# Performance work log

Measured on AMD Instinct MI355X. Metric: run time of the kernel, lower is better.

## Reference

```python
import jax, jax.numpy as jnp
import numpy as np

B, N, D, K, DSPACE, NFREQ = 4, 4096, 256, 16, 3, 5
BN_EPS = 1e-5


def setup_inputs() -> dict:
    key = jax.random.key(0)
    ks = jax.random.split(key, 12)
    s = 1.0 / np.sqrt(D)
    pe_in = DSPACE * 2 * NFREQ + DSPACE  # 33
    return {
        "xyz": jax.random.normal(ks[0], (B, N, DSPACE), jnp.float32),
        "feats": jax.random.normal(ks[1], (B, N, D), jnp.float32),
        "w_q": jax.random.uniform(ks[2], (D, D), jnp.float32, -s, s),
        "w_k": jax.random.uniform(ks[3], (D, D), jnp.float32, -s, s),
        "w_v": jax.random.uniform(ks[4], (D, D), jnp.float32, -s, s),
        "g_w1": jax.random.uniform(ks[5], (D, D), jnp.float32, -s, s),
        "g_b1": jax.random.uniform(ks[6], (D,), jnp.float32, -s, s),
        "g_w2": jax.random.uniform(ks[7], (D, D), jnp.float32, -s, s),
        "g_b2": jax.random.uniform(ks[8], (D,), jnp.float32, -s, s),
        "pe_w": jax.random.uniform(ks[9], (D, pe_in), jnp.float32, -s, s),
        "pe_b": jax.random.uniform(ks[10], (D,), jnp.float32, -s, s),
        "bn_w": jnp.ones((D,), jnp.float32),
        "bn_b": jnp.zeros((D,), jnp.float32),
    }


def _gather_knn(points, idx):
    # points [b,n,c], idx [b,n,k] -> [b,n,k,c]
    return jax.vmap(lambda p, i: p[i])(points, idx)


def reference(xyz, feats, w_q, w_k, w_v, g_w1, g_b1, g_w2, g_b2, pe_w, pe_b, bn_w, bn_b):
    # KNN (no grad in original): full pairwise sq-distance + top-k smallest
    dists = jnp.sum((xyz[:, :, None] - xyz[:, None]) ** 2, axis=-1)  # [b,n,n]
    _, knn_idx = jax.lax.top_k(-dists, K)  # [b,n,k], ascending distance
    knn_idx = jax.lax.stop_gradient(knn_idx)
    knn_xyz = jax.lax.stop_gradient(_gather_knn(xyz, knn_idx))  # [b,n,k,3]

    q = feats @ w_q.T                               # [b,n,d]
    k_g = _gather_knn(feats @ w_k.T, knn_idx)       # [b,n,k,d]
    v_g = _gather_knn(feats @ w_v.T, knn_idx)       # [b,n,k,d]

    pos_diff = xyz[:, :, None] - knn_xyz            # [b,n,k,3]
    freqs = jnp.linspace(1.0, 2.0 ** NFREQ, NFREQ).astype(pos_diff.dtype)
    embeds = [pos_diff]
    for f in freqs:
        embeds.append(jnp.sin(pos_diff * f))
        embeds.append(jnp.cos(pos_diff * f))
    pos_embed = jnp.concatenate(embeds, axis=-1)    # [b,n,k,33]
    pos_encode = pos_embed @ pe_w.T + pe_b          # [b,n,k,d]

    edges = q[:, :, None] - k_g + pos_encode        # [b,n,k,d]
    h = jax.nn.relu(edges @ g_w1.T + g_b1)
    attn = h @ g_w2.T + g_b2                        # [b,n,k,d]
    attn = jax.nn.softmax(attn, axis=-2)            # softmax over neighbors

    res = jnp.einsum('bnkf,bnkf->bnf', attn, v_g + pos_encode) + feats

    # BatchNorm1d over channel dim, training-mode batch stats (biased var)
    mean = jnp.mean(res, axis=(0, 1))
    var = jnp.var(res, axis=(0, 1))
    res = (res - mean) * jax.lax.rsqrt(var + BN_EPS) * bn_w + bn_b
    return res
```

## Files before the change

### kernel.cpp

```cpp
#include <hip/hip_runtime.h>

#define BB 4
#define NN 4096
#define DD 256
#define KK 16
#define PTS 2

typedef __bf16 bf16;
typedef __attribute__((ext_vector_type(8))) __bf16 bf16x8;
typedef __attribute__((ext_vector_type(4))) __bf16 bf16x4;
typedef __attribute__((ext_vector_type(4))) float f32x4;

__global__ __launch_bounds__(256) void prep_kernel(
    const float* __restrict__ wq, const float* __restrict__ wk,
    const float* __restrict__ wv, const float* __restrict__ w1,
    const float* __restrict__ w2, const float* __restrict__ pw,
    bf16* __restrict__ wqb, bf16* __restrict__ wkb, bf16* __restrict__ wvb,
    bf16* __restrict__ w1b, bf16* __restrict__ w2b, bf16* __restrict__ pwb) {
  const int idx = blockIdx.x * 256 + threadIdx.x;
  wqb[idx] = (bf16)wq[idx];
  wkb[idx] = (bf16)wk[idx];
  wvb[idx] = (bf16)wv[idx];
  w1b[idx] = (bf16)w1[idx];
  w2b[idx] = (bf16)w2[idx];
  if (idx < 256 * 64) {
    const int n = idx >> 6, c = idx & 63;
    pwb[idx] = (c < 33) ? (bf16)pw[n * 33 + c] : (bf16)0.f;
  }
}

__global__ __launch_bounds__(256, 2) void knn_v2(const float* __restrict__ xyz,
                                                 int* __restrict__ knn) {
  const int lane = threadIdx.x & 63;
  const int wv = threadIdx.x >> 6;
  const int row = blockIdx.x * 4 + wv;
  const int b = row >> 12, i = row & (NN - 1);
  const float* xb = xyz + (size_t)b * NN * 3;
  const float xi = xb[i * 3 + 0], yi = xb[i * 3 + 1], zi = xb[i * 3 + 2];
  unsigned long long cand[64];
#pragma unroll
  for (int c = 0; c < 64; ++c) {
    const int j = c * 64 + lane;
    const float dx = xi - xb[j * 3 + 0];
    const float dy = yi - xb[j * 3 + 1];
    const float dz = zi - xb[j * 3 + 2];
    const float d = dx * dx + dy * dy + dz * dz;
    const unsigned long long fb = (unsigned long long)(__float_as_uint(d)) + 1ull;
    cand[c] = (fb << 32) | (unsigned int)j;
  }
  unsigned long long lastkey = 0ull;
  unsigned int myj = 0u;
  for (int r = 0; r < KK; ++r) {
    unsigned long long lmin = ~0ull;
#pragma unroll
    for (int c = 0; c < 64; ++c) {
      const unsigned long long v = cand[c];
      if (v > lastkey && v < lmin) lmin = v;
    }
#pragma unroll
    for (int off = 1; off < 64; off <<= 1) {
      const unsigned long long o = __shfl_xor(lmin, off);
      if (o < lmin) lmin = o;
    }
    if (lane == r) myj = (unsigned int)lmin;
    lastkey = lmin;
  }
  if (lane < KK) knn[row * KK + lane] = (int)myj;
}

__global__ __launch_bounds__(256, 4) void proj_mfma(
    const float* __restrict__ feats, const bf16* __restrict__ wqb,
    const bf16* __restrict__ wkb, const bf16* __restrict__ wvb,
    float* __restrict__ q, bf16* __restrict__ kfb, bf16* __restrict__ vfb) {
  const int t = threadIdx.x;
  const int lane = t & 63, wv = t >> 6;
  const int m = lane & 15, qd = lane >> 4;
  const size_t r0 = (size_t)blockIdx.x * 64;
  __shared__ __align__(16) bf16 fs[64][264];
  const float4* f4 = (const float4*)(feats + r0 * DD);
  for (int i = 0; i < 16; ++i) {
    const int e = i * 256 + t;
    const float4 v = f4[e];
    bf16x4 w;
    w[0] = (bf16)v.x; w[1] = (bf16)v.y; w[2] = (bf16)v.z; w[3] = (bf16)v.w;
    *(bf16x4*)&fs[e >> 6][(e & 63) * 4] = w;
  }
  __syncthreads();
  bf16x8 afrag[8];
#pragma unroll
  for (int f = 0; f < 8; ++f)
    afrag[f] = *(const bf16x8*)&fs[wv * 16 + m][f * 32 + qd * 8];
  const bf16* wmat[3] = {wqb, wkb, wvb};
  for (int mat = 0; mat < 3; ++mat) {
    const bf16* wb = wmat[mat];
    for (int nt = 0; nt < 16; ++nt) {
      const int n = nt * 16 + m;
      bf16x8 bfr[8];
#pragma unroll
      for (int f = 0; f < 8; ++f)
        bfr[f] = *(const bf16x8*)(wb + (size_t)n * DD + f * 32 + qd * 8);
      f32x4 c = {0.f, 0.f, 0.f, 0.f};
#pragma unroll
      for (int f = 0; f < 8; ++f)
        c = __builtin_amdgcn_mfma_f32_16x16x32_bf16(afrag[f], bfr[f], c, 0, 0, 0);
#pragma unroll
      for (int rr = 0; rr < 4; ++rr) {
        const size_t o = (r0 + wv * 16 + qd * 4 + rr) * DD + n;
        if (mat == 0) q[o] = c[rr];
        else if (mat == 1) kfb[o] = (bf16)c[rr];
        else vfb[o] = (bf16)c[rr];
      }
    }
  }
}

__global__ __launch_bounds__(256, 3) void edge_v3(
    const float* __restrict__ xyz, const float* __restrict__ feats,
    const float* __restrict__ q, const bf16* __restrict__ kfb,
    const bf16* __restrict__ vfb, const int* __restrict__ knn,
    const bf16* __restrict__ w1b, const float* __restrict__ g_b1,
    const bf16* __restrict__ w2b, const float* __restrict__ g_b2,
    const bf16* __restrict__ pwb, const float* __restrict__ pe_b,
    float* __restrict__ res) {
  const int t = threadIdx.x;
  const int lane = t & 63;
  const int wv = t >> 6;
  const int m = lane & 15;
  const int qd = lane >> 4;
  const int row0 = blockIdx.x * PTS;
  const int b = row0 >> 12;

  __shared__ __align__(16) bf16 emb_s[PTS][16][88];
  __shared__ __align__(16) bf16 bufA[PTS][16][264];
  __shared__ __align__(16) bf16 bufB[PTS][16][264];
  __shared__ int js_s[PTS][16];

  if (t < PTS * 16) js_s[t >> 4][t & 15] = knn[(row0 + (t >> 4)) * KK + (t & 15)];
  __syncthreads();

  const float* xb = xyz + (size_t)b * NN * 3;
  for (int p = 0; p < PTS; ++p) {
    const int i = (row0 + p) & (NN - 1);
    for (int e = t; e < 16 * 88; e += 256) {
      const int k = e / 88, c = e % 88;
      float val = 0.f;
      if (c < 33) {
        const int cc = (c < 3) ? c : (c - 3) % 3;
        const float pd = xb[i * 3 + cc] - xb[js_s[p][k] * 3 + cc];
        if (c < 3) {
          val = pd;
        } else {
          const int f = (c - 3) / 6;
          const float x = pd * fmaf(7.75f, (float)f, 1.0f);
          val = (((c - 3) % 6) < 3) ? __sinf(x) : __cosf(x);
        }
      }
      emb_s[p][k][c] = (bf16)val;
    }
  }
  __syncthreads();

  float vpe[4][PTS][4];
#pragma unroll
  for (int tt = 0; tt < 4; ++tt) {
    const int n = wv * 64 + tt * 16 + m;
    const bf16x8 b0 = *(const bf16x8*)(pwb + (size_t)n * 64 + qd * 8);
    const bf16x8 b1 = *(const bf16x8*)(pwb + (size_t)n * 64 + 32 + qd * 8);
    const float bias = pe_b[n];
#pragma unroll
    for (int p = 0; p < PTS; ++p) {
      const bf16x8 a0 = *(const bf16x8*)&emb_s[p][m][qd * 8];
      const bf16x8 a1 = *(const bf16x8*)&emb_s[p][m][32 + qd * 8];
      f32x4 c = {bias, bias, bias, bias};
      c = __builtin_amdgcn_mfma_f32_16x16x32_bf16(a0, b0, c, 0, 0, 0);
      c = __builtin_amdgcn_mfma_f32_16x16x32_bf16(a1, b1, c, 0, 0, 0);
      const float qv = q[(size_t)(row0 + p) * DD + n];
#pragma unroll
      for (int rr = 0; rr < 4; ++rr) {
        const int krow = qd * 4 + rr;
        const size_t jr = ((size_t)(b * NN + js_s[p][krow])) * DD + n;
        bufA[p][krow][n] = (bf16)(qv - (float)kfb[jr] + c[rr]);
        vpe[tt][p][rr] = (float)vfb[jr] + c[rr];
      }
    }
  }
  __syncthreads();

  {
    bf16x8 afrag[PTS][8];
#pragma unroll
    for (int p = 0; p < PTS; ++p)
#pragma unroll
      for (int f = 0; f < 8; ++f)
        afrag[p][f] = *(const bf16x8*)&bufA[p][m][f * 32 + qd * 8];
    for (int tt = 0; tt < 4; ++tt) {
      const int n = wv * 64 + tt * 16 + m;
      bf16x8 bfr[8];
#pragma unroll
      for (int f = 0; f < 8; ++f)
        bfr[f] = *(const bf16x8*)(w1b + (size_t)n * DD + f * 32 + qd * 8);
      const float bias = g_b1[n];
#pragma unroll
      for (int p = 0; p < PTS; ++p) {
        f32x4 c = {bias, bias, bias, bias};
#pragma unroll
        for (int f = 0; f < 8; ++f)
          c = __builtin_amdgcn_mfma_f32_16x16x32_bf16(afrag[p][f], bfr[f], c, 0, 0, 0);
#pragma unroll
        for (int rr = 0; rr < 4; ++rr)
          bufB[p][qd * 4 + rr][n] = (bf16)fmaxf(c[rr], 0.f);
      }
    }
  }
  __syncthreads();

  {
    bf16x8 afrag[PTS][8];
#pragma unroll
    for (int p = 0; p < PTS; ++p)
#pragma unroll
      for (int f = 0; f < 8; ++f)
        afrag[p][f] = *(const bf16x8*)&bufB[p][m][f * 32 + qd * 8];
#pragma unroll
    for (int tt = 0; tt < 4; ++tt) {
      const int n = wv * 64 + tt * 16 + m;
      bf16x8 bfr[8];
#pragma unroll
      for (int f = 0; f < 8; ++f)
        bfr[f] = *(const bf16x8*)(w2b + (size_t)n * DD + f * 32 + qd * 8);
      const float bias = g_b2[n];
#pragma unroll
      for (int p = 0; p < PTS; ++p) {
        f32x4 c = {bias, bias, bias, bias};
#pragma unroll
        for (int f = 0; f < 8; ++f)
          c = __builtin_amdgcn_mfma_f32_16x16x32_bf16(afrag[p][f], bfr[f], c, 0, 0, 0);
        float mx = fmaxf(fmaxf(c[0], c[1]), fmaxf(c[2], c[3]));
        mx = fmaxf(mx, __shfl_xor(mx, 16));
        mx = fmaxf(mx, __shfl_xor(mx, 32));
        float e[4], den = 0.f;
#pragma unroll
        for (int rr = 0; rr < 4; ++rr) {
          e[rr] = __expf(c[rr] - mx);
          den += e[rr];
        }
        den += __shfl_xor(den, 16);
        den += __shfl_xor(den, 32);
        float num = 0.f;
#pragma unroll
        for (int rr = 0; rr < 4; ++rr) num += e[rr] * vpe[tt][p][rr];
        num += __shfl_xor(num, 16);
        num += __shfl_xor(num, 32);
        if (qd == 0) {
          const size_t o = (size_t)(row0 + p) * DD + n;
          res[o] = num / den + feats[o];
        }
      }
    }
  }
}

__global__ __launch_bounds__(256) void bn_stats(const float* __restrict__ res,
                                                float* __restrict__ sums,
                                                float* __restrict__ sumsq) {
  const int t = threadIdx.x;
  const size_t r0 = (size_t)blockIdx.x * 32;
  float s = 0.f, s2 = 0.f;
  for (int r = 0; r < 32; ++r) {
    const float v = res[(r0 + r) * DD + t];
    s += v;
    s2 += v * v;
  }
  atomicAdd(&sums[t], s);
  atomicAdd(&sumsq[t], s2);
}

__global__ __launch_bounds__(256) void bn_apply(float* __restrict__ out,
                                                const float* __restrict__ sums,
                                                const float* __restrict__ sumsq,
                                                const float* __restrict__ bn_w,
                                                const float* __restrict__ bn_b) {
  const int idx = blockIdx.x * 256 + threadIdx.x;
  const int c = idx & (DD - 1);
  const float inv_n = 1.f / (float)(BB * NN);
  const float mean = sums[c] * inv_n;
  const float var = sumsq[c] * inv_n - mean * mean;
  const float v = out[idx];
  out[idx] = (v - mean) * rsqrtf(var + 1e-5f) * bn_w[c] + bn_b[c];
}

extern "C" void kernel_launch(void* const* d_in, const int* in_sizes, int n_in,
                              void* d_out, int out_size, void* d_ws,
                              size_t ws_size, hipStream_t stream) {
  (void)in_sizes; (void)n_in; (void)out_size; (void)ws_size;
  const float* xyz = (const float*)d_in[0];
  const float* feats = (const float*)d_in[1];
  const float* w_q = (const float*)d_in[2];
  const float* w_k = (const float*)d_in[3];
  const float* w_v = (const float*)d_in[4];
  const float* g_w1 = (const float*)d_in[5];
  const float* g_b1 = (const float*)d_in[6];
  const float* g_w2 = (const float*)d_in[7];
  const float* g_b2 = (const float*)d_in[8];
  const float* pe_w = (const float*)d_in[9];
  const float* pe_b = (const float*)d_in[10];
  const float* bn_w = (const float*)d_in[11];
  const float* bn_b = (const float*)d_in[12];
  float* out = (float*)d_out;

  const int BN = BB * NN;
  char* w = (char*)d_ws;
  int* knn = (int*)w;       w += (size_t)BN * KK * 4;
  float* q = (float*)w;     w += (size_t)BN * DD * 4;
  bf16* kfb = (bf16*)w;     w += (size_t)BN * DD * 2;
  bf16* vfb = (bf16*)w;     w += (size_t)BN * DD * 2;
  float* sums = (float*)w;  w += DD * 4;
  float* sumsq = (float*)w; w += DD * 4;
  bf16* wqb = (bf16*)w;     w += (size_t)DD * DD * 2;
  bf16* wkb = (bf16*)w;     w += (size_t)DD * DD * 2;
  bf16* wvb = (bf16*)w;     w += (size_t)DD * DD * 2;
  bf16* w1b = (bf16*)w;     w += (size_t)DD * DD * 2;
  bf16* w2b = (bf16*)w;     w += (size_t)DD * DD * 2;
  bf16* pwb = (bf16*)w;     w += (size_t)DD * 64 * 2;

  prep_kernel<<<DD * DD / 256, 256, 0, stream>>>(w_q, w_k, w_v, g_w1, g_w2,
                                                 pe_w, wqb, wkb, wvb, w1b, w2b,
                                                 pwb);
  knn_v2<<<BN / 4, 256, 0, stream>>>(xyz, knn);
  proj_mfma<<<BN / 64, 256, 0, stream>>>(feats, wqb, wkb, wvb, q, kfb, vfb);
  edge_v3<<<BN / PTS, 256, 0, stream>>>(xyz, feats, q, kfb, vfb, knn, w1b, g_b1,
                                        w2b, g_b2, pwb, pe_b, out);
  hipMemsetAsync(sums, 0, 2 * DD * sizeof(float), stream);
  bn_stats<<<BN / 32, 256, 0, stream>>>(out, sums, sumsq);
  bn_apply<<<BN, 256, 0, stream>>>(out, sums, sumsq, bn_w, bn_b);
}
```

Before: 679.5 us.

## Prefetch gathered K/V rows into registers early and alias edge LDS buffers

The edge kernel now issues the gathered key and value loads right after reading the neighbour indices. Keys are loaded as row-contiguous bf16x8 MFMA A-fragments straight from global memory, and the q-k+pe subtraction happens in registers, so the bufA round trip is gone. The embedding buffer and the hidden-activation buffer share one LDS region, which cuts shared-memory use, and the sums memset moves into the prep kernel to drop one launch. In exchange, register pressure rises because the ab and vpe arrays stay live across the positional-encoding stage, which could reduce occupancy under launch_bounds(256,3).

New measurement: 762.6 us. 1.12x slower.

```diff
diff --git a/kernel.cpp b/kernel.cpp
--- a/kernel.cpp
+++ b/kernel.cpp
@@ -16,7 +16,8 @@
     const float* __restrict__ wv, const float* __restrict__ w1,
     const float* __restrict__ w2, const float* __restrict__ pw,
     bf16* __restrict__ wqb, bf16* __restrict__ wkb, bf16* __restrict__ wvb,
-    bf16* __restrict__ w1b, bf16* __restrict__ w2b, bf16* __restrict__ pwb) {
+    bf16* __restrict__ w1b, bf16* __restrict__ w2b, bf16* __restrict__ pwb,
+    float* __restrict__ sums) {
   const int idx = blockIdx.x * 256 + threadIdx.x;
   wqb[idx] = (bf16)wq[idx];
   wkb[idx] = (bf16)wk[idx];
@@ -27,6 +28,7 @@
     const int n = idx >> 6, c = idx & 63;
     pwb[idx] = (c < 33) ? (bf16)pw[n * 33 + c] : (bf16)0.f;
   }
+  if (idx < 2 * DD) sums[idx] = 0.f;
 }
 
 __global__ __launch_bounds__(256, 2) void knn_v2(const float* __restrict__ xyz,
@@ -114,7 +116,7 @@
   }
 }
 
-__global__ __launch_bounds__(256, 3) void edge_v3(
+__global__ __launch_bounds__(256, 3) void edge_v4(
     const float* __restrict__ xyz, const float* __restrict__ feats,
     const float* __restrict__ q, const bf16* __restrict__ kfb,
     const bf16* __restrict__ vfb, const int* __restrict__ knn,
@@ -130,37 +132,64 @@
   const int row0 = blockIdx.x * PTS;
   const int b = row0 >> 12;
 
-  __shared__ __align__(16) bf16 emb_s[PTS][16][88];
-  __shared__ __align__(16) bf16 bufA[PTS][16][264];
-  __shared__ __align__(16) bf16 bufB[PTS][16][264];
+  __shared__ __align__(16) bf16 peq_s[PTS][16][264];
+  __shared__ __align__(16) char un_s[PTS * 16 * 264 * 2];
+  bf16(*hs)[16][264] = (bf16(*)[16][264])un_s;
+  bf16(*emb_s)[16][96] = (bf16(*)[16][96])un_s;
   __shared__ int js_s[PTS][16];
 
   if (t < PTS * 16) js_s[t >> 4][t & 15] = knn[(row0 + (t >> 4)) * KK + (t & 15)];
   __syncthreads();
 
+  float vpe[4][PTS][4];
+#pragma unroll
+  for (int tt = 0; tt < 4; ++tt) {
+    const int n = wv * 64 + tt * 16 + m;
+#pragma unroll
+    for (int p = 0; p < PTS; ++p)
+#pragma unroll
+      for (int rr = 0; rr < 4; ++rr)
+        vpe[tt][p][rr] =
+            (float)vfb[((size_t)(b * NN + js_s[p][qd * 4 + rr])) * DD + n];
+  }
+  bf16x8 ab[PTS][8];
+#pragma unroll
+  for (int p = 0; p < PTS; ++p) {
+    const size_t base = ((size_t)(b * NN + js_s[p][m])) * DD;
+#pragma unroll
+    for (int f = 0; f < 8; ++f)
+      ab[p][f] = *(const bf16x8*)(kfb + base + f * 32 + qd * 8);
+  }
+
   const float* xb = xyz + (size_t)b * NN * 3;
-  for (int p = 0; p < PTS; ++p) {
-    const int i = (row0 + p) & (NN - 1);
-    for (int e = t; e < 16 * 88; e += 256) {
-      const int k = e / 88, c = e % 88;
-      float val = 0.f;
-      if (c < 33) {
-        const int cc = (c < 3) ? c : (c - 3) % 3;
-        const float pd = xb[i * 3 + cc] - xb[js_s[p][k] * 3 + cc];
-        if (c < 3) {
-          val = pd;
-        } else {
-          const int f = (c - 3) / 6;
-          const float x = pd * fmaf(7.75f, (float)f, 1.0f);
-          val = (((c - 3) % 6) < 3) ? __sinf(x) : __cosf(x);
+  {
+    const int k = t >> 4;
+    const int c0 = (t & 15) * 6;
+#pragma unroll
+    for (int p = 0; p < PTS; ++p) {
+      const int i = (row0 + p) & (NN - 1);
+      const int j = js_s[p][k];
+#pragma unroll
+      for (int cc = 0; cc < 6; ++cc) {
+        const int c = c0 + cc;
+        float val = 0.f;
+        if (c < 33) {
+          const int ax = (c < 3) ? c : (c - 3) % 3;
+          const float pd = xb[i * 3 + ax] - xb[j * 3 + ax];
+          if (c < 3) {
+            val = pd;
+          } else {
+            const int f = (c - 3) / 6;
+            const float x = pd * fmaf(7.75f, (float)f, 1.0f);
+            val = (((c - 3) % 6) < 3) ? __sinf(x) : __cosf(x);
+          }
         }
-      }
-      emb_s[p][k][c] = (bf16)val;
-    }
-  }
-  __syncthreads();
-
-  float vpe[4][PTS][4];
+        emb_s[p][k][c] = (bf16)val;
+      }
+    }
+  }
+  __syncthreads();
+
 #pragma unroll
   for (int tt = 0; tt < 4; ++tt) {
     const int n = wv * 64 + tt * 16 + m;
@@ -177,84 +206,82 @@
       const float qv = q[(size_t)(row0 + p) * DD + n];
 #pragma unroll
       for (int rr = 0; rr < 4; ++rr) {
-        const int krow = qd * 4 + rr;
-        const size_t jr = ((size_t)(b * NN + js_s[p][krow])) * DD + n;
-        bufA[p][krow][n] = (bf16)(qv - (float)kfb[jr] + c[rr]);
-        vpe[tt][p][rr] = (float)vfb[jr] + c[rr];
-      }
-    }
-  }
-  __syncthreads();
-
-  {
-    bf16x8 afrag[PTS][8];
-#pragma unroll
-    for (int p = 0; p < PTS; ++p)
+        peq_s[p][qd * 4 + rr][n] = (bf16)(c[rr] + qv);
+        vpe[tt][p][rr] += c[rr];
+      }
+    }
+  }
+  __syncthreads();
+
+#pragma unroll
+  for (int p = 0; p < PTS; ++p) {
+#pragma unroll
+    for (int f = 0; f < 8; ++f) {
+      const bf16x8 pq = *(const bf16x8*)&peq_s[p][m][f * 32 + qd * 8];
+      bf16x8 e;
+#pragma unroll
+      for (int x = 0; x < 8; ++x) e[x] = (bf16)((float)pq[x] - (float)ab[p][f][x]);
+      ab[p][f] = e;
+    }
+  }
+  for (int tt = 0; tt < 4; ++tt) {
+    const int n = wv * 64 + tt * 16 + m;
+    bf16x8 bfr[8];
+#pragma unroll
+    for (int f = 0; f < 8; ++f)
+      bfr[f] = *(const bf16x8*)(w1b + (size_t)n * DD + f * 32 + qd * 8);
+    const float bias = g_b1[n];
+#pragma unroll
+    for (int p = 0; p < PTS; ++p) {
+      f32x4 c = {bias, bias, bias, bias};
 #pragma unroll
       for (int f = 0; f < 8; ++f)
-        afrag[p][f] = *(const bf16x8*)&bufA[p][m][f * 32 + qd * 8];
-    for (int tt = 0; tt < 4; ++tt) {
-      const int n = wv * 64 + tt * 16 + m;
-      bf16x8 bfr[8];
+        c = __builtin_amdgcn_mfma_f32_16x16x32_bf16(ab[p][f], bfr[f], c, 0, 0, 0);
+#pragma unroll
+      for (int rr = 0; rr < 4; ++rr)
+        hs[p][qd * 4 + rr][n] = (bf16)fmaxf(c[rr], 0.f);
+    }
+  }
+  __syncthreads();
+
+#pragma unroll
+  for (int p = 0; p < PTS; ++p)
+#pragma unroll
+    for (int f = 0; f < 8; ++f)
+      ab[p][f] = *(const bf16x8*)&hs[p][m][f * 32 + qd * 8];
+#pragma unroll
+  for (int tt = 0; tt < 4; ++tt) {
+    const int n = wv * 64 + tt * 16 + m;
+    bf16x8 bfr[8];
+#pragma unroll
+    for (int f = 0; f < 8; ++f)
+      bfr[f] = *(const bf16x8*)(w2b + (size_t)n * DD + f * 32 + qd * 8);
+    const float bias = g_b2[n];
+#pragma unroll
+    for (int p = 0; p < PTS; ++p) {
+      f32x4 c = {bias, bias, bias, bias};
 #pragma unroll
       for (int f = 0; f < 8; ++f)
-        bfr[f] = *(const bf16x8*)(w1b + (size_t)n * DD + f * 32 + qd * 8);
-      const float bias = g_b1[n];
-#pragma unroll
-      for (int p = 0; p < PTS; ++p) {
-        f32x4 c = {bias, bias, bias, bias};
-#pragma unroll
-        for (int f = 0; f < 8; ++f)
-          c = __builtin_amdgcn_mfma_f32_16x16x32_bf16(afrag[p][f], bfr[f], c, 0, 0, 0);
-#pragma unroll
-        for (int rr = 0; rr < 4; ++rr)
-          bufB[p][qd * 4 + rr][n] = (bf16)fmaxf(c[rr], 0.f);
-      }
-    }
-  }
-  __syncthreads();
-
-  {
-    bf16x8 afrag[PTS][8];
-#pragma unroll
-    for (int p = 0; p < PTS; ++p)
-#pragma unroll
-      for (int f = 0; f < 8; ++f)
-        afrag[p][f] = *(const bf16x8*)&bufB[p][m][f * 32 + qd * 8];
-#pragma unroll
-    for (int tt = 0; tt < 4; ++tt) {
-      const int n = wv * 64 + tt * 16 + m;
-      bf16x8 bfr[8];
-#pragma unroll
-      for (int f = 0; f < 8; ++f)
-        bfr[f] = *(const bf16x8*)(w2b + (size_t)n * DD + f * 32 + qd * 8);
-      const float bias = g_b2[n];
-#pragma unroll
-      for (int p = 0; p < PTS; ++p) {
-        f32x4 c = {bias, bias, bias, bias};
-#pragma unroll
-        for (int f = 0; f < 8; ++f)
-          c = __builtin_amdgcn_mfma_f32_16x16x32_bf16(afrag[p][f], bfr[f], c, 0, 0, 0);
-        float mx = fmaxf(fmaxf(c[0], c[1]), fmaxf(c[2], c[3]));
-        mx = fmaxf(mx, __shfl_xor(mx, 16));
-        mx = fmaxf(mx, __shfl_xor(mx, 32));
-        float e[4], den = 0.f;
-#pragma unroll
-        for (int rr = 0; rr < 4; ++rr) {
-          e[rr] = __expf(c[rr] - mx);
-          den += e[rr];
-        }
-        den += __shfl_xor(den, 16);
-        den += __shfl_xor(den, 32);
-        float num = 0.f;
-#pragma unroll
-        for (int rr = 0; rr < 4; ++rr) num += e[rr] * vpe[tt][p][rr];
-        num += __shfl_xor(num, 16);
-        num += __shfl_xor(num, 32);
-        if (qd == 0) {
-          const size_t o = (size_t)(row0 + p) * DD + n;
-          res[o] = num / den + feats[o];
-        }
+        c = __builtin_amdgcn_mfma_f32_16x16x32_bf16(ab[p][f], bfr[f], c, 0, 0, 0);
+      float mx = fmaxf(fmaxf(c[0], c[1]), fmaxf(c[2], c[3]));
+      mx = fmaxf(mx, __shfl_xor(mx, 16));
+      mx = fmaxf(mx, __shfl_xor(mx, 32));
+      float e[4], den = 0.f;
+#pragma unroll
+      for (int rr = 0; rr < 4; ++rr) {
+        e[rr] = __expf(c[rr] - mx);
+        den += e[rr];
+      }
+      den += __shfl_xor(den, 16);
+      den += __shfl_xor(den, 32);
+      float num = 0.f;
+#pragma unroll
+      for (int rr = 0; rr < 4; ++rr) num += e[rr] * vpe[tt][p][rr];
+      num += __shfl_xor(num, 16);
+      num += __shfl_xor(num, 32);
+      if (qd == 0) {
+        const size_t o = (size_t)(row0 + p) * DD + n;
+        res[o] = num / den + feats[o];
       }
     }
   }
@@ -325,12 +352,11 @@
 
   prep_kernel<<<DD * DD / 256, 256, 0, stream>>>(w_q, w_k, w_v, g_w1, g_w2,
                                                  pe_w, wqb, wkb, wvb, w1b, w2b,
-                                                 pwb);
+                                                 pwb, sums);
   knn_v2<<<BN / 4, 256, 0, stream>>>(xyz, knn);
   proj_mfma<<<BN / 64, 256, 0, stream>>>(feats, wqb, wkb, wvb, q, kfb, vfb);
-  edge_v3<<<BN / PTS, 256, 0, stream>>>(xyz, feats, q, kfb, vfb, knn, w1b, g_b1,
+  edge_v4<<<BN / PTS, 256, 0, stream>>>(xyz, feats, q, kfb, vfb, knn, w1b, g_b1,
                                         w2b, g_b2, pwb, pe_b, out);
-  hipMemsetAsync(sums, 0, 2 * DD * sizeof(float), stream);
   bn_stats<<<BN / 32, 256, 0, stream>>>(out, sums, sumsq);
   bn_apply<<<BN, 256, 0, stream>>>(out, sums, sumsq, bn_w, bn_b);
 }
```
